# Kernel optimization log

Measured on AMD Instinct MI355X. Metric: run time of the kernel, lower is better.

Reference implementation:

```python
import jax, jax.numpy as jnp
import numpy as np

B, N, S, C_IN = 8, 1024, 64, 1
H = 32  # hidden_ch


def _mpnn(W, b, x, g):
    # Faithful to MPNN(concat_h=False): messages[b,c,m,n] = x[b,c,m] * g[b,n,m],
    # flattened to (c m) channels and hit by a 1x1 conv W of shape (H, c, m).
    # out[b,u,n] = sum_{c,m} W[u,c,m] * x[b,c,m] * g[b,n,m] + b[u]
    t = jnp.einsum('ucm,bcm->bum', W, x)          # tiny contraction over c
    return jnp.einsum('bum,bnm->bun', t, g) + b[None, :, None]


def setup_inputs() -> dict:
    key = jax.random.key(0)
    ks = jax.random.split(key, 14)
    gate_scale = 1.0 / np.sqrt(C_IN * N)

    def gate_w(k):
        return jax.random.normal(k, (H, C_IN, N), jnp.float32) * gate_scale

    return {
        'x': jax.random.normal(ks[0], (B, N, S, C_IN), jnp.float32),
        'mask': jnp.ones((B, N, S, C_IN), dtype=bool),  # unused by the module
        'fwd_graph': jax.random.uniform(ks[1], (B, N, N), jnp.float32),
        # GRU gate MPNN 1x1-conv weights, reshaped (H, C_IN*N, 1) -> (H, C_IN, N)
        'Wf': gate_w(ks[2]), 'bf': jnp.zeros((H,), jnp.float32),
        'Wu': gate_w(ks[3]), 'bu': jnp.zeros((H,), jnp.float32),
        'Wc': gate_w(ks[4]), 'bc': jnp.zeros((H,), jnp.float32),
        'h0': jnp.zeros((H, N), jnp.float32),
        'W1': jax.random.normal(ks[5], (H, H), jnp.float32) / np.sqrt(H),
        'b1': jnp.zeros((H,), jnp.float32),
        'W2': jax.random.normal(ks[6], (H, 2 * H), jnp.float32) / np.sqrt(2 * H),
        'b2': jnp.zeros((H,), jnp.float32),
        # LocalConv1D: per-node 1x1 conv, weights (n, out_ch, 2H), bias (n, out_ch)
        'Wd': jax.random.normal(ks[7], (N, C_IN, 2 * H), jnp.float32) / np.sqrt(2 * H),
        'bd': jnp.zeros((N, C_IN), jnp.float32),
    }


def reference(x, mask, fwd_graph, Wf, bf, Wu, bu, Wc, bc, h0, W1, b1, W2, b2, Wd, bd):
    del mask  # present in the torch signature but never used
    b = x.shape[0]
    xs = jnp.transpose(x, (2, 0, 3, 1))  # (s, b, c, n)
    g = fwd_graph
    h_init = jnp.broadcast_to(h0[None], (b, H, N))

    def step(h, x_t):
        # NOTE: with concat_h=False the forget gate r = sigmoid(MPNN_f(x)) only
        # rescales h passed into c_gate, which ignores h entirely -> r (Wf, bf)
        # has no effect on the output; omitted here (same math).
        u = jax.nn.sigmoid(_mpnn(Wu, bu, x_t, g))
        c = jnp.tanh(_mpnn(Wc, bc, x_t, g))
        h_new = u * h + (1.0 - u) * c
        return h_new, None

    h, _ = jax.lax.scan(step, h_init, xs)

    # Prediction head (only the last step's prediction is returned: pred[:, :, -1:])
    x1 = jax.nn.leaky_relu(jnp.einsum('uh,bhn->bun', W1, h) + b1[None, :, None])
    x2 = jax.nn.leaky_relu(
        jnp.einsum('uk,bkn->bun', W2, jnp.concatenate([x1, h], axis=1)) + b2[None, :, None])
    dec_in = jnp.concatenate([x2, h], axis=1)  # (b, 2H, n)
    # LocalConv1D (per-node weights), fully batched:
    x_hat = jnp.einsum('nok,bkn->bon', Wd, dec_in) + bd.T[None, :, :]  # (b, c, n)
    return jnp.transpose(x_hat, (0, 2, 1))[:, :, None, :]  # (b, n, 1, c)
```

## Files before the change

kernel.cpp:

```cpp
#include <hip/hip_runtime.h>
#include <hip/hip_bf16.h>
#include <hip/hip_fp16.h>

#define Bsz 8
#define Nn 1024
#define Ss 64
#define Hh 32

typedef _Float16 half8 __attribute__((ext_vector_type(8)));
typedef _Float16 half4 __attribute__((ext_vector_type(4)));
typedef float f32x4 __attribute__((ext_vector_type(4)));

__device__ __forceinline__ void gload_lds16(const _Float16* g, _Float16* l) {
  __builtin_amdgcn_global_load_lds(
      (const __attribute__((address_space(1))) unsigned int*)g,
      (__attribute__((address_space(3))) unsigned int*)l, 16, 0, 0);
}

__global__ __launch_bounds__(256)
void prep(const float* __restrict__ x, const float* __restrict__ Wu,
          const float* __restrict__ Wc, const float* __restrict__ g,
          _Float16* __restrict__ xT, _Float16* __restrict__ Wh,
          _Float16* __restrict__ gh) {
  const int tid = threadIdx.x;
  if (blockIdx.x < 64) {
    const int b = blockIdx.x >> 3;
    const int m0 = (blockIdx.x & 7) * 128;
    __shared__ _Float16 tile[128 * 68];
    const int m = tid >> 1;
    const int hf = tid & 1;
    const float* src = x + ((size_t)(b * Nn + m0 + m)) * Ss + hf * 32;
#pragma unroll
    for (int i = 0; i < 8; ++i) {
      const float4 v = *(const float4*)(src + i * 4);
      half4 o;
      o[0] = (_Float16)v.x; o[1] = (_Float16)v.y;
      o[2] = (_Float16)v.z; o[3] = (_Float16)v.w;
      *(half4*)(&tile[m * 68 + hf * 32 + i * 4]) = o;
    }
    __syncthreads();
    const int t = tid & 63;
    const int q = tid >> 6;
    _Float16* dst = xT + ((size_t)(b * 64 + t)) * Nn + m0 + q * 32;
#pragma unroll
    for (int i = 0; i < 4; ++i) {
      half8 o;
#pragma unroll
      for (int e = 0; e < 8; ++e) o[e] = tile[(q * 32 + i * 8 + e) * 68 + t];
      *(half8*)(dst + i * 8) = o;
    }
  } else if (blockIdx.x < 72) {
    const int w = blockIdx.x - 64;
    const size_t i0 = ((size_t)(w * 256 + tid)) * 32;
#pragma unroll
    for (int i = 0; i < 8; ++i) {
      const size_t i4 = i0 + i * 4;
      const float* s = (i4 < 32768) ? (Wu + i4) : (Wc + (i4 - 32768));
      const float4 v = *(const float4*)s;
      half4 o;
      o[0] = (_Float16)v.x; o[1] = (_Float16)v.y;
      o[2] = (_Float16)v.z; o[3] = (_Float16)v.w;
      *(half4*)(&Wh[i4]) = o;
    }
  } else {
    const size_t i = ((size_t)(blockIdx.x - 72) * 256 + tid) * 4;
    const float4 v = *(const float4*)(&g[i]);
    half4 o;
    o[0] = (_Float16)v.x; o[1] = (_Float16)v.y;
    o[2] = (_Float16)v.z; o[3] = (_Float16)v.w;
    *(half4*)(&gh[i]) = o;
  }
}

__global__ __launch_bounds__(256)
void gemm_recur(const _Float16* __restrict__ xT, const _Float16* __restrict__ Wh,
                const _Float16* __restrict__ G, const float* __restrict__ bu,
                const float* __restrict__ bc, const float* __restrict__ h0,
                float* __restrict__ H) {
  __shared__ __align__(16) char smem[32768];
  _Float16* Xs = (_Float16*)smem;
  _Float16* Gs = (_Float16*)(smem + 4096);
  _Float16* Cs = (_Float16*)smem;

  const int u = blockIdx.x;
  const int col0 = blockIdx.y * 128;
  const int b = blockIdx.z;
  const int tid = threadIdx.x;
  const int lane = tid & 63;
  const int wave = tid >> 6;
  const int wr = (wave >> 1) * 64;
  const int wc = (wave & 1) * 64;
  const int gate = wave >> 1;

  const _Float16* Xb = xT + (size_t)b * 64 * Nn;
  const _Float16* Gb = G + ((size_t)b * Nn + col0) * Nn;
  const _Float16* Wg = Wh + ((size_t)gate * 32 + u) * Nn;

  f32x4 acc[4][4] = {};

  const int srow = lane >> 2;
  const int scol = (lane & 3) * 8;
  const int koff = (lane >> 4) * 8;

  for (int kk = 0; kk < 32; ++kk) {
    const int k0 = kk * 32;
    gload_lds16(Xb + (size_t)(wave * 16 + srow) * Nn + k0 + scol,
                Xs + wave * 512);
#pragma unroll
    for (int i = 0; i < 2; ++i) {
      const int chunk = wave * 2 + i;
      gload_lds16(Gb + (size_t)(chunk * 16 + srow) * Nn + k0 + scol,
                  Gs + chunk * 512);
    }
    const half8 wv = *(const half8*)(Wg + k0 + koff);
    __syncthreads();

    half8 af[4], bf[4];
#pragma unroll
    for (int mi = 0; mi < 4; ++mi) {
      const half8 x8 = *(const half8*)(&Xs[(mi * 16 + (lane & 15)) * 32 + koff]);
      af[mi] = wv * x8;
    }
#pragma unroll
    for (int ni = 0; ni < 4; ++ni)
      bf[ni] = *(const half8*)(&Gs[(wc + ni * 16 + (lane & 15)) * 32 + koff]);
#pragma unroll
    for (int mi = 0; mi < 4; ++mi)
#pragma unroll
      for (int ni = 0; ni < 4; ++ni)
        acc[mi][ni] = __builtin_amdgcn_mfma_f32_16x16x32_f16(af[mi], bf[ni], acc[mi][ni], 0, 0, 0);
    __syncthreads();
  }

#pragma unroll
  for (int mi = 0; mi < 4; ++mi)
#pragma unroll
    for (int ni = 0; ni < 4; ++ni)
#pragma unroll
      for (int j = 0; j < 4; ++j) {
        const int r = wr + mi * 16 + (lane >> 4) * 4 + j;
        const int c = wc + ni * 16 + (lane & 15);
        Cs[r * 128 + (c ^ (((r >> 2) & 3) << 3))] = (_Float16)acc[mi][ni][j];
      }
  __syncthreads();

  if (tid < 128) {
    const int n = col0 + tid;
    const float bias_u = bu[u];
    const float bias_c = bc[u];
    float h = h0[u * Nn + n];
    for (int t = 0; t < 64; ++t) {
      const int cc = tid ^ (((t >> 2) & 3) << 3);
      const float yu = (float)Cs[t * 128 + cc] + bias_u;
      const float yc = (float)Cs[(64 + t) * 128 + cc] + bias_c;
      const float s = 1.f / (1.f + __expf(-yu));
      const float e = __expf(-2.f * fabsf(yc));
      float th = (1.f - e) / (1.f + e);
      th = yc < 0.f ? -th : th;
      h = s * h + (1.f - s) * th;
    }
    H[((size_t)b * Hh + u) * Nn + n] = h;
  }
}

__global__ __launch_bounds__(128)
void head(const float* __restrict__ H, const float* __restrict__ W1,
          const float* __restrict__ b1, const float* __restrict__ W2,
          const float* __restrict__ b2, const float* __restrict__ Wd,
          const float* __restrict__ bd, float* __restrict__ out) {
  const int b = blockIdx.x >> 3;
  const int n = (blockIdx.x & 7) * 128 + threadIdx.x;
  const float* Hb = H + (size_t)b * Hh * Nn;
  float h[32];
#pragma unroll
  for (int u = 0; u < 32; ++u) h[u] = Hb[u * Nn + n];
  float x1[32];
#pragma unroll 4
  for (int v = 0; v < 32; ++v) {
    float a = b1[v];
#pragma unroll
    for (int u = 0; u < 32; ++u) a += W1[v * 32 + u] * h[u];
    x1[v] = a > 0.f ? a : 0.01f * a;
  }
  float x2[32];
#pragma unroll 4
  for (int v = 0; v < 32; ++v) {
    float a = b2[v];
#pragma unroll
    for (int u = 0; u < 32; ++u) a += W2[v * 64 + u] * x1[u];
#pragma unroll
    for (int u = 0; u < 32; ++u) a += W2[v * 64 + 32 + u] * h[u];
    x2[v] = a > 0.f ? a : 0.01f * a;
  }
  float o = bd[n];
#pragma unroll
  for (int v = 0; v < 32; ++v) o += Wd[n * 64 + v] * x2[v];
#pragma unroll
  for (int v = 0; v < 32; ++v) o += Wd[n * 64 + 32 + v] * h[v];
  out[(size_t)b * Nn + n] = o;
}

extern "C" void kernel_launch(void* const* d_in, const int* in_sizes, int n_in,
                              void* d_out, int out_size, void* d_ws, size_t ws_size,
                              hipStream_t stream) {
  const float* x  = (const float*)d_in[0];
  const float* g  = (const float*)d_in[2];
  const float* Wu = (const float*)d_in[5];
  const float* bu = (const float*)d_in[6];
  const float* Wc = (const float*)d_in[7];
  const float* bc = (const float*)d_in[8];
  const float* h0 = (const float*)d_in[9];
  const float* W1 = (const float*)d_in[10];
  const float* b1 = (const float*)d_in[11];
  const float* W2 = (const float*)d_in[12];
  const float* b2 = (const float*)d_in[13];
  const float* Wd = (const float*)d_in[14];
  const float* bd = (const float*)d_in[15];
  float* out = (float*)d_out;

  char* ws = (char*)d_ws;
  _Float16* xT = (_Float16*)(ws);
  _Float16* Wh = (_Float16*)(ws + (size_t)(1u << 20));
  _Float16* gh = (_Float16*)(ws + (size_t)(2u << 20));
  float*    Hx = (float*)  (ws + (size_t)(18u << 20));

  prep<<<72 + 8192, 256, 0, stream>>>(x, Wu, Wc, g, xT, Wh, gh);
  dim3 gg(32, 8, 8);
  gemm_recur<<<gg, 256, 0, stream>>>(xT, Wh, gh, bu, bc, h0, Hx);
  head<<<64, 128, 0, stream>>>(Hx, W1, b1, W2, b2, Wd, bd, out);
}
```

Baseline: 234.9 us.

## Double-buffer LDS tiles, swizzle LDS layout, and remap blocks for XCD locality

```diff
diff --git a/kernel.cpp b/kernel.cpp
--- a/kernel.cpp
+++ b/kernel.cpp
@@ -78,59 +78,74 @@
                 const float* __restrict__ bc, const float* __restrict__ h0,
                 float* __restrict__ H) {
   __shared__ __align__(16) char smem[32768];
-  _Float16* Xs = (_Float16*)smem;
-  _Float16* Gs = (_Float16*)(smem + 4096);
+  _Float16* X0 = (_Float16*)smem;
+  _Float16* G0 = (_Float16*)(smem + 4096);
+  _Float16* X1 = (_Float16*)(smem + 12288);
+  _Float16* G1 = (_Float16*)(smem + 16384);
   _Float16* Cs = (_Float16*)smem;
 
-  const int u = blockIdx.x;
-  const int col0 = blockIdx.y * 128;
-  const int b = blockIdx.z;
+  const int id = blockIdx.x;
+  const int wg = (id & 7) * 256 + (id >> 3);
+  const int u = wg & 31;
+  const int col0 = ((wg >> 5) & 7) * 128;
+  const int b = wg >> 8;
+
   const int tid = threadIdx.x;
   const int lane = tid & 63;
   const int wave = tid >> 6;
-  const int wr = (wave >> 1) * 64;
+  const int gate = wave >> 1;
+  const int wr = gate * 64;
   const int wc = (wave & 1) * 64;
-  const int gate = wave >> 1;
+  const int l15 = lane & 15;
+  const int s = lane >> 4;
 
   const _Float16* Xb = xT + (size_t)b * 64 * Nn;
   const _Float16* Gb = G + ((size_t)b * Nn + col0) * Nn;
   const _Float16* Wg = Wh + ((size_t)gate * 32 + u) * Nn;
 
+  const int srow = lane >> 2;
+  const int ssw = ((lane & 3) ^ ((lane >> 3) & 3)) * 8;
+  const int ps8 = (s ^ ((l15 >> 1) & 3)) * 8;
+
   f32x4 acc[4][4] = {};
 
-  const int srow = lane >> 2;
-  const int scol = (lane & 3) * 8;
-  const int koff = (lane >> 4) * 8;
-
-  for (int kk = 0; kk < 32; ++kk) {
-    const int k0 = kk * 32;
-    gload_lds16(Xb + (size_t)(wave * 16 + srow) * Nn + k0 + scol,
-                Xs + wave * 512);
-#pragma unroll
-    for (int i = 0; i < 2; ++i) {
-      const int chunk = wave * 2 + i;
-      gload_lds16(Gb + (size_t)(chunk * 16 + srow) * Nn + k0 + scol,
-                  Gs + chunk * 512);
-    }
-    const half8 wv = *(const half8*)(Wg + k0 + koff);
+#define STAGE(k0, Xd, Gd)                                                    \
+  do {                                                                       \
+    gload_lds16(Xb + (size_t)(wave * 16 + srow) * Nn + (k0) + ssw,           \
+                (Xd) + wave * 512);                                          \
+    gload_lds16(Gb + (size_t)(wave * 32 + srow) * Nn + (k0) + ssw,           \
+                (Gd) + wave * 1024);                                         \
+    gload_lds16(Gb + (size_t)(wave * 32 + 16 + srow) * Nn + (k0) + ssw,      \
+                (Gd) + wave * 1024 + 512);                                   \
+  } while (0)
+
+#define COMPUTE(k0, Xd, Gd)                                                  \
+  do {                                                                       \
+    const half8 wv = *(const half8*)(Wg + (k0) + s * 8);                     \
+    half8 af[4], bf[4];                                                      \
+    _Pragma("unroll") for (int mi = 0; mi < 4; ++mi)                         \
+        af[mi] = *(const half8*)(&(Xd)[(mi * 16 + l15) * 32 + ps8]) * wv;    \
+    _Pragma("unroll") for (int ni = 0; ni < 4; ++ni)                         \
+        bf[ni] = *(const half8*)(&(Gd)[(wc + ni * 16 + l15) * 32 + ps8]);    \
+    _Pragma("unroll") for (int mi = 0; mi < 4; ++mi)                         \
+      _Pragma("unroll") for (int ni = 0; ni < 4; ++ni)                       \
+          acc[mi][ni] = __builtin_amdgcn_mfma_f32_16x16x32_f16(              \
+              af[mi], bf[ni], acc[mi][ni], 0, 0, 0);                         \
+  } while (0)
+
+  STAGE(0, X0, G0);
+  __syncthreads();
+#pragma unroll 2
+  for (int kk = 0; kk < 32; kk += 2) {
+    STAGE((kk + 1) * 32, X1, G1);
+    COMPUTE(kk * 32, X0, G0);
     __syncthreads();
-
-    half8 af[4], bf[4];
-#pragma unroll
-    for (int mi = 0; mi < 4; ++mi) {
-      const half8 x8 = *(const half8*)(&Xs[(mi * 16 + (lane & 15)) * 32 + koff]);
-      af[mi] = wv * x8;
-    }
-#pragma unroll
-    for (int ni = 0; ni < 4; ++ni)
-      bf[ni] = *(const half8*)(&Gs[(wc + ni * 16 + (lane & 15)) * 32 + koff]);
-#pragma unroll
-    for (int mi = 0; mi < 4; ++mi)
-#pragma unroll
-      for (int ni = 0; ni < 4; ++ni)
-        acc[mi][ni] = __builtin_amdgcn_mfma_f32_16x16x32_f16(af[mi], bf[ni], acc[mi][ni], 0, 0, 0);
+    if (kk < 30) STAGE((kk + 2) * 32, X0, G0);
+    COMPUTE((kk + 1) * 32, X1, G1);
     __syncthreads();
   }
+#undef STAGE
+#undef COMPUTE
 
 #pragma unroll
   for (int mi = 0; mi < 4; ++mi)
@@ -139,7 +154,7 @@
 #pragma unroll
       for (int j = 0; j < 4; ++j) {
         const int r = wr + mi * 16 + (lane >> 4) * 4 + j;
-        const int c = wc + ni * 16 + (lane & 15);
+        const int c = wc + ni * 16 + l15;
         Cs[r * 128 + (c ^ (((r >> 2) & 3) << 3))] = (_Float16)acc[mi][ni][j];
       }
   __syncthreads();
@@ -153,11 +168,11 @@
       const int cc = tid ^ (((t >> 2) & 3) << 3);
       const float yu = (float)Cs[t * 128 + cc] + bias_u;
       const float yc = (float)Cs[(64 + t) * 128 + cc] + bias_c;
-      const float s = 1.f / (1.f + __expf(-yu));
+      const float sg = 1.f / (1.f + __expf(-yu));
       const float e = __expf(-2.f * fabsf(yc));
       float th = (1.f - e) / (1.f + e);
       th = yc < 0.f ? -th : th;
-      h = s * h + (1.f - s) * th;
+      h = sg * h + (1.f - sg) * th;
     }
     H[((size_t)b * Hh + u) * Nn + n] = h;
   }
@@ -225,7 +240,6 @@
   float*    Hx = (float*)  (ws + (size_t)(18u << 20));
 
   prep<<<72 + 8192, 256, 0, stream>>>(x, Wu, Wc, g, xT, Wh, gh);
-  dim3 gg(32, 8, 8);
-  gemm_recur<<<gg, 256, 0, stream>>>(xT, Wh, gh, bu, bc, h0, Hx);
+  gemm_recur<<<2048, 256, 0, stream>>>(xT, Wh, gh, bu, bc, h0, Hx);
   head<<<64, 128, 0, stream>>>(Hx, W1, b1, W2, b2, Wd, bd, out);
 }
```

New measurement: 249.1 us. +6.1%, slower.

## Halve GEMM column tile, swizzle LDS layout, remap blocks for XCD locality

Applied to the files above, without the earlier changes.

```diff
diff --git a/kernel.cpp b/kernel.cpp
--- a/kernel.cpp
+++ b/kernel.cpp
@@ -77,57 +77,53 @@
                 const _Float16* __restrict__ G, const float* __restrict__ bu,
                 const float* __restrict__ bc, const float* __restrict__ h0,
                 float* __restrict__ H) {
-  __shared__ __align__(16) char smem[32768];
+  __shared__ __align__(16) char smem[16384];
   _Float16* Xs = (_Float16*)smem;
   _Float16* Gs = (_Float16*)(smem + 4096);
   _Float16* Cs = (_Float16*)smem;
 
-  const int u = blockIdx.x;
-  const int col0 = blockIdx.y * 128;
-  const int b = blockIdx.z;
+  const int id = blockIdx.x;
+  const int wg = (id & 7) * 512 + (id >> 3);
+  const int u = wg & 31;
+  const int col0 = ((wg >> 5) & 15) * 64;
+  const int b = wg >> 9;
+
   const int tid = threadIdx.x;
   const int lane = tid & 63;
   const int wave = tid >> 6;
-  const int wr = (wave >> 1) * 64;
-  const int wc = (wave & 1) * 64;
   const int gate = wave >> 1;
+  const int wc = (wave & 1) * 32;
+  const int l15 = lane & 15;
+  const int s = lane >> 4;
 
   const _Float16* Xb = xT + (size_t)b * 64 * Nn;
   const _Float16* Gb = G + ((size_t)b * Nn + col0) * Nn;
   const _Float16* Wg = Wh + ((size_t)gate * 32 + u) * Nn;
 
-  f32x4 acc[4][4] = {};
-
   const int srow = lane >> 2;
-  const int scol = (lane & 3) * 8;
-  const int koff = (lane >> 4) * 8;
+  const int ssw = ((lane & 3) ^ ((lane >> 3) & 3)) * 8;
+  const int ps8 = (s ^ ((l15 >> 1) & 3)) * 8;
+
+  f32x4 acc[4][2] = {};
 
   for (int kk = 0; kk < 32; ++kk) {
     const int k0 = kk * 32;
-    gload_lds16(Xb + (size_t)(wave * 16 + srow) * Nn + k0 + scol,
-                Xs + wave * 512);
-#pragma unroll
-    for (int i = 0; i < 2; ++i) {
-      const int chunk = wave * 2 + i;
-      gload_lds16(Gb + (size_t)(chunk * 16 + srow) * Nn + k0 + scol,
-                  Gs + chunk * 512);
-    }
-    const half8 wv = *(const half8*)(Wg + k0 + koff);
+    gload_lds16(Xb + (size_t)(wave * 16 + srow) * Nn + k0 + ssw, Xs + wave * 512);
+    gload_lds16(Gb + (size_t)(wave * 16 + srow) * Nn + k0 + ssw, Gs + wave * 512);
+    const half8 wv = *(const half8*)(Wg + k0 + s * 8);
     __syncthreads();
 
-    half8 af[4], bf[4];
-#pragma unroll
-    for (int mi = 0; mi < 4; ++mi) {
-      const half8 x8 = *(const half8*)(&Xs[(mi * 16 + (lane & 15)) * 32 + koff]);
-      af[mi] = wv * x8;
-    }
-#pragma unroll
-    for (int ni = 0; ni < 4; ++ni)
-      bf[ni] = *(const half8*)(&Gs[(wc + ni * 16 + (lane & 15)) * 32 + koff]);
+    half8 af[4], bf[2];
 #pragma unroll
     for (int mi = 0; mi < 4; ++mi)
-#pragma unroll
-      for (int ni = 0; ni < 4; ++ni)
+      af[mi] = *(const half8*)(&Xs[(mi * 16 + l15) * 32 + ps8]) * wv;
+#pragma unroll
+    for (int ni = 0; ni < 2; ++ni)
+      bf[ni] = *(const half8*)(&Gs[(wc + ni * 16 + l15) * 32 + ps8]);
+#pragma unroll
+    for (int mi = 0; mi < 4; ++mi)
+#pragma unroll
+      for (int ni = 0; ni < 2; ++ni)
         acc[mi][ni] = __builtin_amdgcn_mfma_f32_16x16x32_f16(af[mi], bf[ni], acc[mi][ni], 0, 0, 0);
     __syncthreads();
   }
@@ -135,29 +131,29 @@
 #pragma unroll
   for (int mi = 0; mi < 4; ++mi)
 #pragma unroll
-    for (int ni = 0; ni < 4; ++ni)
+    for (int ni = 0; ni < 2; ++ni)
 #pragma unroll
       for (int j = 0; j < 4; ++j) {
-        const int r = wr + mi * 16 + (lane >> 4) * 4 + j;
-        const int c = wc + ni * 16 + (lane & 15);
-        Cs[r * 128 + (c ^ (((r >> 2) & 3) << 3))] = (_Float16)acc[mi][ni][j];
+        const int r = gate * 64 + mi * 16 + (lane >> 4) * 4 + j;
+        const int c = wc + ni * 16 + l15;
+        Cs[r * 64 + (c ^ (((r >> 2) & 3) << 3))] = (_Float16)acc[mi][ni][j];
       }
   __syncthreads();
 
-  if (tid < 128) {
+  if (tid < 64) {
     const int n = col0 + tid;
     const float bias_u = bu[u];
     const float bias_c = bc[u];
     float h = h0[u * Nn + n];
     for (int t = 0; t < 64; ++t) {
       const int cc = tid ^ (((t >> 2) & 3) << 3);
-      const float yu = (float)Cs[t * 128 + cc] + bias_u;
-      const float yc = (float)Cs[(64 + t) * 128 + cc] + bias_c;
-      const float s = 1.f / (1.f + __expf(-yu));
+      const float yu = (float)Cs[t * 64 + cc] + bias_u;
+      const float yc = (float)Cs[(64 + t) * 64 + cc] + bias_c;
+      const float sg = 1.f / (1.f + __expf(-yu));
       const float e = __expf(-2.f * fabsf(yc));
       float th = (1.f - e) / (1.f + e);
       th = yc < 0.f ? -th : th;
-      h = s * h + (1.f - s) * th;
+      h = sg * h + (1.f - sg) * th;
     }
     H[((size_t)b * Hh + u) * Nn + n] = h;
   }
@@ -225,7 +221,6 @@
   float*    Hx = (float*)  (ws + (size_t)(18u << 20));
 
   prep<<<72 + 8192, 256, 0, stream>>>(x, Wu, Wc, g, xT, Wh, gh);
-  dim3 gg(32, 8, 8);
-  gemm_recur<<<gg, 256, 0, stream>>>(xT, Wh, gh, bu, bc, h0, Hx);
+  gemm_recur<<<4096, 256, 0, stream>>>(xT, Wh, gh, bu, bc, h0, Hx);
   head<<<64, 128, 0, stream>>>(Hx, W1, b1, W2, b2, Wd, bd, out);
 }
```

Measured after the change: 241.2 us. +2.7%, slower.
